# Kernel optimization log

Measured on AMD Instinct MI355X. Metric: run time of the kernel, lower is better.

Reference implementation:

```python
import jax, jax.numpy as jnp
import numpy as np

N_POWER_ITER = 5


def _spectral_normalize(w, n_iter=N_POWER_ITER):
    # w: [out, in] 1x1-conv weight; divide by top singular value (power iteration,
    # deterministic init), mirroring torch.nn.utils.spectral_norm's reparameterization.
    u = jnp.full((w.shape[0],), 1.0 / np.sqrt(w.shape[0]), dtype=w.dtype)
    for _ in range(n_iter):
        v = w.T @ u
        v = v / (jnp.linalg.norm(v) + 1e-12)
        u = w @ v
        u = u / (jnp.linalg.norm(u) + 1e-12)
    sigma = u @ (w @ v)
    return w / sigma


def _maxpool2x2(x):
    # x: [B, C, H, W] -> [B, C, H//2, W//2]
    B, C, H, W = x.shape
    return x.reshape(B, C, H // 2, 2, W // 2, 2).max(axis=(3, 5))


def _conv1x1(w, x):
    # 1x1 conv == channel-mixing einsum. w: [out, in], x: [B, in, H, W]
    return jnp.einsum('oc,bchw->bohw', w, x)


def setup_inputs() -> dict:
    key = jax.random.key(0)
    kx, kq, kk, kv, ko = jax.random.split(key, 5)
    C = 512
    B, H, W = 16, 64, 64
    scale = 0.05
    return {
        'x': jax.random.normal(kx, (B, C, H, W), dtype=jnp.float32),
        'Wq': jax.random.normal(kq, (C // 8, C), dtype=jnp.float32) * scale,
        'Wk': jax.random.normal(kk, (C // 8, C), dtype=jnp.float32) * scale,
        'Wv': jax.random.normal(kv, (C // 2, C), dtype=jnp.float32) * scale,
        'Wo': jax.random.normal(ko, (C, C // 2), dtype=jnp.float32) * scale,
        'gamma': jnp.array([0.5], dtype=jnp.float32),
    }


def reference(x, Wq, Wk, Wv, Wo, gamma):
    B, C, H, W = x.shape
    n_ftrs = H * W
    wq = _spectral_normalize(Wq)
    wk = _spectral_normalize(Wk)
    wv = _spectral_normalize(Wv)
    wo = _spectral_normalize(Wo)
    f = _conv1x1(wq, x).reshape(B, C // 8, n_ftrs)                      # [B, C/8, HW]
    g = _maxpool2x2(_conv1x1(wk, x)).reshape(B, C // 8, n_ftrs // 4)    # [B, C/8, HW/4]
    h = _maxpool2x2(_conv1x1(wv, x)).reshape(B, C // 2, n_ftrs // 4)    # [B, C/2, HW/4]
    # scores: [B, HW, HW/4]; softmax over kv positions
    beta = jax.nn.softmax(jnp.einsum('bcn,bcm->bnm', f, g), axis=-1)
    # attention output: [B, C/2, HW]
    o = jnp.einsum('bcm,bnm->bcn', h, beta).reshape(B, C // 2, H, W)
    o = _conv1x1(wo, o)                                                 # [B, C, H, W]
    return gamma.reshape(()) * o + x
```

## Files before the change

kernel.cpp:

```cpp
#include <hip/hip_runtime.h>
#include <cstdint>

typedef __attribute__((ext_vector_type(8))) short bf16x8;
typedef __attribute__((ext_vector_type(4))) float f32x4;
typedef __attribute__((ext_vector_type(2))) unsigned int u32x2;

#define B_   16
#define C_   512
#define HW_  4096
#define M3_  384
#define HWP_ 1024
#define CV_  256

__device__ __forceinline__ unsigned short f2b(float f) {
  union { float f; unsigned u; } v; v.f = f;
  unsigned r = v.u + 0x7fffu + ((v.u >> 16) & 1u);
  return (unsigned short)(r >> 16);
}
__device__ __forceinline__ float b2f(unsigned short b) {
  union { unsigned u; float f; } v; v.u = ((unsigned)b) << 16;
  return v.f;
}
__device__ __forceinline__ f32x4 mfma16(bf16x8 a, bf16x8 b, f32x4 c) {
  return __builtin_amdgcn_mfma_f32_16x16x32_bf16(a, b, c, 0, 0, 0);
}

__global__ __launch_bounds__(256) void k_transpose(const float* __restrict__ x,
                                                   unsigned short* __restrict__ xb) {
  __shared__ unsigned short t[64][66];
  const int b = blockIdx.z, k0 = blockIdx.y * 64, n0 = blockIdx.x * 64;
  const float* xp = x + (size_t)b * C_ * HW_;
  const int ln = threadIdx.x & 63, g = threadIdx.x >> 6;
  for (int kk = g; kk < 64; kk += 4)
    t[kk][ln] = f2b(xp[(size_t)(k0 + kk) * HW_ + n0 + ln]);
  __syncthreads();
  unsigned short* xo = xb + (size_t)b * HW_ * C_;
  for (int nn = g; nn < 64; nn += 4)
    xo[(size_t)(n0 + nn) * C_ + k0 + ln] = t[ln][nn];
}

__global__ __launch_bounds__(256) void k_wtrans(
    const float* __restrict__ Wq, const float* __restrict__ Wk,
    const float* __restrict__ Wv, const float* __restrict__ Wo,
    float* __restrict__ wt) {
  const float* w; int out, in; float* dst;
  switch (blockIdx.z) {
    case 0: w = Wq; out = 64;  in = 512; dst = wt;          break;
    case 1: w = Wk; out = 64;  in = 512; dst = wt + 32768;  break;
    case 2: w = Wv; out = 256; in = 512; dst = wt + 65536;  break;
    default: w = Wo; out = 512; in = 256; dst = wt + 196608; break;
  }
  const int o0 = blockIdx.y * 64, i0 = blockIdx.x * 64;
  if (o0 >= out || i0 >= in) return;
  __shared__ float t[64][65];
  const int ln = threadIdx.x & 63, g = threadIdx.x >> 6;
  for (int oo = g; oo < 64; oo += 4)
    t[oo][ln] = w[(size_t)(o0 + oo) * in + i0 + ln];
  __syncthreads();
  for (int ii = g; ii < 64; ii += 4)
    dst[(size_t)(i0 + ii) * out + o0 + ln] = t[ln][ii];
}

__device__ __forceinline__ float breduce1024(float val, float* red) {
  __syncthreads();
#pragma unroll
  for (int off = 32; off > 0; off >>= 1) val += __shfl_down(val, off);
  if ((threadIdx.x & 63) == 0) red[threadIdx.x >> 6] = val;
  __syncthreads();
  float s = 0.f;
#pragma unroll
  for (int i = 0; i < 16; ++i) s += red[i];
  return s;
}

__global__ __launch_bounds__(1024) void k_specnorm(
    const float* __restrict__ Wq, const float* __restrict__ Wk,
    const float* __restrict__ Wv, const float* __restrict__ Wo,
    const float* __restrict__ wt,
    unsigned short* __restrict__ wqkv, unsigned short* __restrict__ wob) {
  __shared__ float u[512], v[512];
  __shared__ float part[4096];
  __shared__ float red[16];
  const float* w; const float* wT; int out, in; unsigned short* dst;
  switch (blockIdx.x) {
    case 0: w = Wq; wT = wt;          out = 64;  in = 512; dst = wqkv;             break;
    case 1: w = Wk; wT = wt + 32768;  out = 64;  in = 512; dst = wqkv + 64 * 512;  break;
    case 2: w = Wv; wT = wt + 65536;  out = 256; in = 512; dst = wqkv + 128 * 512; break;
    default: w = Wo; wT = wt + 196608; out = 512; in = 256; dst = wob;             break;
  }
  const int tid = threadIdx.x;
  const float rs = rsqrtf((float)out);
  if (tid < out) u[tid] = rs;
  __syncthreads();
  for (int it = 0; it < 5; ++it) {
    {
      const int G = in >> 2, nch = 1024 / G;
      const int ch = tid / G, grp = tid - ch * G;
      const int rpc = out / nch, obase = ch * rpc;
      f32x4 acc = {0.f, 0.f, 0.f, 0.f};
#pragma unroll 8
      for (int r = 0; r < rpc; ++r) {
        const int o = obase + r;
        const f32x4 wv = *reinterpret_cast<const f32x4*>(&w[(size_t)o * in + grp * 4]);
        const float uo = u[o];
        acc[0] += wv[0] * uo; acc[1] += wv[1] * uo;
        acc[2] += wv[2] * uo; acc[3] += wv[3] * uo;
      }
      *reinterpret_cast<f32x4*>(&part[ch * in + grp * 4]) = acc;
      __syncthreads();
      if (tid < in) {
        float s = 0.f;
        for (int c2 = 0; c2 < nch; ++c2) s += part[c2 * in + tid];
        v[tid] = s;
      }
    }
    {
      float ss = 0.f;
      __syncthreads();
      if (tid < in) ss = v[tid] * v[tid];
      ss = breduce1024(ss, red);
      const float sv = 1.f / (sqrtf(ss) + 1e-12f);
      if (tid < in) v[tid] *= sv;
      __syncthreads();
    }
    {
      const int G = out >> 2, nch = 1024 / G;
      const int ch = tid / G, grp = tid - ch * G;
      const int cpc = in / nch, cbase = ch * cpc;
      f32x4 acc = {0.f, 0.f, 0.f, 0.f};
#pragma unroll 8
      for (int r = 0; r < cpc; ++r) {
        const int c = cbase + r;
        const f32x4 wv = *reinterpret_cast<const f32x4*>(&wT[(size_t)c * out + grp * 4]);
        const float vc = v[c];
        acc[0] += wv[0] * vc; acc[1] += wv[1] * vc;
        acc[2] += wv[2] * vc; acc[3] += wv[3] * vc;
      }
      *reinterpret_cast<f32x4*>(&part[ch * out + grp * 4]) = acc;
      __syncthreads();
      if (tid < out) {
        float s = 0.f;
        for (int c2 = 0; c2 < nch; ++c2) s += part[c2 * out + tid];
        u[tid] = s;
      }
    }
    {
      float su = 0.f;
      __syncthreads();
      if (tid < out) su = u[tid] * u[tid];
      su = breduce1024(su, red);
      const float sv2 = 1.f / (sqrtf(su) + 1e-12f);
      if (tid < out) u[tid] *= sv2;
      __syncthreads();
    }
  }
  float sp = 0.f;
  {
    const int G = out >> 2, nch = 1024 / G;
    const int ch = tid / G, grp = tid - ch * G;
    const int cpc = in / nch, cbase = ch * cpc;
    f32x4 acc = {0.f, 0.f, 0.f, 0.f};
#pragma unroll 8
    for (int r = 0; r < cpc; ++r) {
      const int c = cbase + r;
      const f32x4 wv = *reinterpret_cast<const f32x4*>(&wT[(size_t)c * out + grp * 4]);
      const float vc = v[c];
      acc[0] += wv[0] * vc; acc[1] += wv[1] * vc;
      acc[2] += wv[2] * vc; acc[3] += wv[3] * vc;
    }
    *reinterpret_cast<f32x4*>(&part[ch * out + grp * 4]) = acc;
    __syncthreads();
    if (tid < out) {
      float s = 0.f;
      for (int c2 = 0; c2 < nch; ++c2) s += part[c2 * out + tid];
      sp = s * u[tid];
    }
  }
  sp = breduce1024(sp, red);
  const float oscale = (blockIdx.x == 0) ? 1.44269504f : 1.0f;
  const float inv_sigma = (1.f / sp) * oscale;
  const int total = out * in;
  for (int i = tid * 4; i < total; i += 4096) {
    const f32x4 wv = *reinterpret_cast<const f32x4*>(&w[i]);
    u32x2 pw;
    pw[0] = ((unsigned)f2b(wv[1] * inv_sigma) << 16) | f2b(wv[0] * inv_sigma);
    pw[1] = ((unsigned)f2b(wv[3] * inv_sigma) << 16) | f2b(wv[2] * inv_sigma);
    *reinterpret_cast<u32x2*>(&dst[i]) = pw;
  }
}

__global__ __launch_bounds__(256) void k_gemm_qkv(
    const unsigned short* __restrict__ xb, const unsigned short* __restrict__ wqkv,
    unsigned short* __restrict__ yt) {
  __shared__ alignas(16) char smem[32768];
  unsigned short* As = (unsigned short*)smem;
  unsigned short* Bs = (unsigned short*)(smem + 16384);
  const int lid = blockIdx.x;
  const int swz = (lid & 7) * 192 + (lid >> 3);
  const int mt = swz % 3, rest = swz / 3;
  const int nt = rest & 31, b = rest >> 5;
  const int n0 = nt * 128, m0 = mt * 128;
  const unsigned short* Ap = xb + (size_t)b * HW_ * C_ + (size_t)n0 * C_;
  const unsigned short* Bp = wqkv + (size_t)m0 * C_;
  const int tid = threadIdx.x, lane = tid & 63, wid = tid >> 6;
  const int wn = (wid >> 1) * 64, wm = (wid & 1) * 64;
  f32x4 acc[4][4] = {};
  for (int k0 = 0; k0 < C_; k0 += 64) {
    __syncthreads();
#pragma unroll
    for (int i = 0; i < 4; ++i) {
      const int r = i * 32 + (tid >> 3);
      const int s = tid & 7, ss = s ^ (r & 7);
      *reinterpret_cast<f32x4*>(&As[r * 64 + ss * 8]) =
          *reinterpret_cast<const f32x4*>(&Ap[(size_t)r * C_ + k0 + s * 8]);
      *reinterpret_cast<f32x4*>(&Bs[r * 64 + ss * 8]) =
          *reinterpret_cast<const f32x4*>(&Bp[(size_t)r * C_ + k0 + s * 8]);
    }
    __syncthreads();
#pragma unroll
    for (int kk = 0; kk < 2; ++kk) {
      bf16x8 af[4], bfr[4];
#pragma unroll
      for (int i = 0; i < 4; ++i) {
        const int r = wn + i * 16 + (lane & 15);
        const int slot = (kk * 4 + (lane >> 4)) ^ (r & 7);
        af[i] = *reinterpret_cast<const bf16x8*>(&As[r * 64 + slot * 8]);
      }
#pragma unroll
      for (int j = 0; j < 4; ++j) {
        const int r = wm + j * 16 + (lane & 15);
        const int slot = (kk * 4 + (lane >> 4)) ^ (r & 7);
        bfr[j] = *reinterpret_cast<const bf16x8*>(&Bs[r * 64 + slot * 8]);
      }
#pragma unroll
      for (int i = 0; i < 4; ++i)
#pragma unroll
        for (int j = 0; j < 4; ++j) acc[i][j] = mfma16(af[i], bfr[j], acc[i][j]);
    }
  }
  unsigned short* eps = (unsigned short*)smem;
  unsigned short* Y = yt + (size_t)b * HW_ * M3_;
#pragma unroll
  for (int h = 0; h < 2; ++h) {
    __syncthreads();
    if ((wid >> 1) == h) {
#pragma unroll
      for (int i = 0; i < 4; ++i)
#pragma unroll
        for (int j = 0; j < 4; ++j)
#pragma unroll
          for (int r = 0; r < 4; ++r) {
            const int nl = i * 16 + (lane >> 4) * 4 + r;
            const int ml = wm + j * 16 + (lane & 15);
            eps[nl * 136 + ml] = f2b(acc[i][j][r]);
          }
    }
    __syncthreads();
#pragma unroll
    for (int t = 0; t < 4; ++t) {
      const int row = t * 16 + (tid >> 4);
      const int m8 = (tid & 15) * 8;
      *reinterpret_cast<f32x4*>(&Y[(size_t)(n0 + h * 64 + row) * M3_ + m0 + m8]) =
          *reinterpret_cast<const f32x4*>(&eps[row * 136 + m8]);
    }
  }
}

__global__ __launch_bounds__(256) void k_pool_g(const unsigned short* __restrict__ yt,
                                                unsigned short* __restrict__ gt) {
  const int b = blockIdx.y, mp0 = blockIdx.x * 64;
  const int c = threadIdx.x & 63, dm = threadIdx.x >> 6;
  const unsigned short* Y = yt + (size_t)b * HW_ * M3_;
  unsigned short* G = gt + (size_t)b * HWP_ * 64;
  for (int mm = dm; mm < 64; mm += 4) {
    const int mp = mp0 + mm;
    const int n00 = (mp >> 5) * 128 + (mp & 31) * 2;
    const float a0 = b2f(Y[(size_t)n00 * M3_ + 64 + c]);
    const float a1 = b2f(Y[(size_t)(n00 + 1) * M3_ + 64 + c]);
    const float a2 = b2f(Y[(size_t)(n00 + 64) * M3_ + 64 + c]);
    const float a3 = b2f(Y[(size_t)(n00 + 65) * M3_ + 64 + c]);
    G[(size_t)mp * 64 + c] = f2b(fmaxf(fmaxf(a0, a1), fmaxf(a2, a3)));
  }
}

__global__ __launch_bounds__(256) void k_pool_vt(const unsigned short* __restrict__ yt,
                                                 unsigned short* __restrict__ vt) {
  __shared__ unsigned short t[64][66];
  const int b = blockIdx.z, mp0 = blockIdx.x * 64, cv0 = blockIdx.y * 64;
  const unsigned short* Y = yt + (size_t)b * HW_ * M3_;
  const int c = threadIdx.x & 63, dm = threadIdx.x >> 6;
  for (int mm = dm; mm < 64; mm += 4) {
    const int mp = mp0 + mm;
    const int n00 = (mp >> 5) * 128 + (mp & 31) * 2;
    const float a0 = b2f(Y[(size_t)n00 * M3_ + 128 + cv0 + c]);
    const float a1 = b2f(Y[(size_t)(n00 + 1) * M3_ + 128 + cv0 + c]);
    const float a2 = b2f(Y[(size_t)(n00 + 64) * M3_ + 128 + cv0 + c]);
    const float a3 = b2f(Y[(size_t)(n00 + 65) * M3_ + 128 + cv0 + c]);
    t[mm][c] = f2b(fmaxf(fmaxf(a0, a1), fmaxf(a2, a3)));
  }
  __syncthreads();
  unsigned short* V = vt + (size_t)b * CV_ * HWP_;
  for (int cc = dm; cc < 64; cc += 4)
    V[(size_t)(cv0 + cc) * HWP_ + mp0 + c] = t[c][cc];
}

__global__ __launch_bounds__(256, 2) void k_attn(
    const unsigned short* __restrict__ yt, const unsigned short* __restrict__ gt,
    const unsigned short* __restrict__ vt, unsigned short* __restrict__ oat) {
  __shared__ alignas(16) char smem[57344];
  unsigned short* Ks = (unsigned short*)smem;
  unsigned short* Vs = (unsigned short*)(smem + 8192);
  unsigned short* Ps = (unsigned short*)(smem + 40960);
  const int lid = blockIdx.x;
  const int swz = (lid & 7) * 64 + (lid >> 3);
  const int q0 = (swz & 31) * 128, b = swz >> 5;
  const int tid = threadIdx.x, lane = tid & 63, wid = tid >> 6;
  const int q = lane & 15, g = lane >> 4;
  const unsigned short* Qg = yt + (size_t)b * HW_ * M3_ + (size_t)(q0 + wid * 32) * M3_;
  const unsigned short* Gg = gt + (size_t)b * HWP_ * 64;
  const unsigned short* Vg = vt + (size_t)b * CV_ * HWP_;
  unsigned short* P = Ps + wid * 2048;
  bf16x8 qf[2][2];
#pragma unroll
  for (int h = 0; h < 2; ++h)
#pragma unroll
    for (int kk = 0; kk < 2; ++kk)
      qf[h][kk] = *reinterpret_cast<const bf16x8*>(&Qg[(size_t)(h * 16 + q) * M3_ + kk * 32 + g * 8]);
  f32x4 kreg[2], vreg[8];
#pragma unroll
  for (int t = 0; t < 2; ++t) {
    const int i = tid + t * 256, r = i >> 3, s = i & 7;
    kreg[t] = *reinterpret_cast<const f32x4*>(&Gg[(size_t)r * 64 + s * 8]);
  }
#pragma unroll
  for (int t = 0; t < 8; ++t) {
    const int i = tid + t * 256, r = i >> 3, s = i & 7;
    vreg[t] = *reinterpret_cast<const f32x4*>(&Vg[(size_t)r * HWP_ + s * 8]);
  }
  f32x4 oacc[2][16] = {};
  float m_run[2] = {-1e30f, -1e30f}, l_run[2] = {0.f, 0.f};
  for (int it = 0; it < 16; ++it) {
    __syncthreads();
#pragma unroll
    for (int t = 0; t < 2; ++t) {
      const int i = tid + t * 256, r = i >> 3, s = i & 7, ss = s ^ (r & 7);
      *reinterpret_cast<f32x4*>(&Ks[r * 64 + ss * 8]) = kreg[t];
    }
#pragma unroll
    for (int t = 0; t < 8; ++t) {
      const int i = tid + t * 256, r = i >> 3, s = i & 7, ss = s ^ (r & 7);
      *reinterpret_cast<f32x4*>(&Vs[r * 64 + ss * 8]) = vreg[t];
    }
    __syncthreads();
    if (it < 15) {
      const int kvn = (it + 1) * 64;
#pragma unroll
      for (int t = 0; t < 2; ++t) {
        const int i = tid + t * 256, r = i >> 3, s = i & 7;
        kreg[t] = *reinterpret_cast<const f32x4*>(&Gg[(size_t)(kvn + r) * 64 + s * 8]);
      }
#pragma unroll
      for (int t = 0; t < 8; ++t) {
        const int i = tid + t * 256, r = i >> 3, s = i & 7;
        vreg[t] = *reinterpret_cast<const f32x4*>(&Vg[(size_t)r * HWP_ + kvn + s * 8]);
      }
    }
    f32x4 sacc[2][4] = {};
#pragma unroll
    for (int kk = 0; kk < 2; ++kk) {
      bf16x8 kf[4];
#pragma unroll
      for (int i = 0; i < 4; ++i) {
        const int row = i * 16 + q;
        const int sl = (kk * 4 + g) ^ (row & 7);
        kf[i] = *reinterpret_cast<const bf16x8*>(&Ks[row * 64 + sl * 8]);
      }
#pragma unroll
      for (int h = 0; h < 2; ++h)
#pragma unroll
        for (int i = 0; i < 4; ++i) sacc[h][i] = mfma16(kf[i], qf[h][kk], sacc[h][i]);
    }
#pragma unroll
    for (int h = 0; h < 2; ++h) {
      float tmax = -1e30f;
#pragma unroll
      for (int i = 0; i < 4; ++i)
#pragma unroll
        for (int r = 0; r < 4; ++r) tmax = fmaxf(tmax, sacc[h][i][r]);
      tmax = fmaxf(tmax, __shfl_xor(tmax, 16));
      tmax = fmaxf(tmax, __shfl_xor(tmax, 32));
      if (__any(tmax > m_run[h] + 11.0f)) {
        const float mnew = fmaxf(m_run[h], tmax);
        const float alpha = exp2f(m_run[h] - mnew);
        m_run[h] = mnew;
        l_run[h] *= alpha;
        float al[4];
#pragma unroll
        for (int r = 0; r < 4; ++r) al[r] = __shfl(alpha, g * 4 + r);
#pragma unroll
        for (int j = 0; j < 16; ++j) {
          oacc[h][j][0] *= al[0]; oacc[h][j][1] *= al[1];
          oacc[h][j][2] *= al[2]; oacc[h][j][3] *= al[3];
        }
      }
      const int qg = h * 16 + q;
      float lsum = 0.f;
#pragma unroll
      for (int i = 0; i < 4; ++i) {
        const float p0 = exp2f(sacc[h][i][0] - m_run[h]);
        const float p1 = exp2f(sacc[h][i][1] - m_run[h]);
        const float p2 = exp2f(sacc[h][i][2] - m_run[h]);
        const float p3 = exp2f(sacc[h][i][3] - m_run[h]);
        lsum += (p0 + p1) + (p2 + p3);
        u32x2 pw;
        pw[0] = ((unsigned)f2b(p1) << 16) | f2b(p0);
        pw[1] = ((unsigned)f2b(p3) << 16) | f2b(p2);
        const int sl = (2 * i + (g >> 1)) ^ (qg & 7);
        *reinterpret_cast<u32x2*>(&P[qg * 64 + sl * 8 + (g & 1) * 4]) = pw;
      }
      lsum += __shfl_xor(lsum, 16);
      lsum += __shfl_xor(lsum, 32);
      l_run[h] += lsum;
    }
    __builtin_amdgcn_s_setprio(1);
#pragma unroll
    for (int kk = 0; kk < 2; ++kk) {
      bf16x8 pa[2];
#pragma unroll
      for (int h = 0; h < 2; ++h)
        pa[h] = *reinterpret_cast<const bf16x8*>(
            &P[(h * 16 + q) * 64 + (((kk * 4 + g) ^ (q & 7))) * 8]);
#pragma unroll
      for (int j = 0; j < 16; ++j) {
        const int row = j * 16 + q;
        const int sl = (kk * 4 + g) ^ (row & 7);
        const bf16x8 vf = *reinterpret_cast<const bf16x8*>(&Vs[row * 64 + sl * 8]);
        oacc[0][j] = mfma16(pa[0], vf, oacc[0][j]);
        oacc[1][j] = mfma16(pa[1], vf, oacc[1][j]);
      }
    }
    __builtin_amdgcn_s_setprio(0);
  }
  float linv[2][4];
#pragma unroll
  for (int h = 0; h < 2; ++h) {
    const float myinv = 1.f / l_run[h];
#pragma unroll
    for (int r = 0; r < 4; ++r) linv[h][r] = __shfl(myinv, g * 4 + r);
  }
  unsigned short* eps = (unsigned short*)smem;
  unsigned short* O = oat + (size_t)b * HW_ * CV_ + (size_t)q0 * CV_;
#pragma unroll
  for (int ch = 0; ch < 2; ++ch) {
    __syncthreads();
    if ((wid >> 1) == ch) {
#pragma unroll
      for (int h = 0; h < 2; ++h)
#pragma unroll
        for (int j = 0; j < 16; ++j)
#pragma unroll
          for (int r = 0; r < 4; ++r) {
            const int row = (wid & 1) * 32 + h * 16 + g * 4 + r;
            const int cv = j * 16 + q;
            eps[row * 264 + cv] = f2b(oacc[h][j][r] * linv[h][r]);
          }
    }
    __syncthreads();
#pragma unroll
    for (int t = 0; t < 8; ++t) {
      const int row = t * 8 + (tid >> 5);
      const int cv8 = (tid & 31) * 8;
      *reinterpret_cast<f32x4*>(&O[(size_t)(ch * 64 + row) * CV_ + cv8]) =
          *reinterpret_cast<const f32x4*>(&eps[row * 264 + cv8]);
    }
  }
}

__global__ __launch_bounds__(256) void k_gemm_out(
    const unsigned short* __restrict__ oat, const unsigned short* __restrict__ wob,
    const float* __restrict__ x, const float* __restrict__ gamma,
    float* __restrict__ out) {
  __shared__ alignas(16) char smem[32768];
  unsigned short* As = (unsigned short*)smem;
  unsigned short* Bs = (unsigned short*)(smem + 16384);
  const int lid = blockIdx.x;
  const int swz = (lid & 7) * 256 + (lid >> 3);
  const int ct = swz & 3, nt = (swz >> 2) & 31, b = swz >> 7;
  const int n0 = nt * 128, co0 = ct * 128;
  const unsigned short* Ap = wob + (size_t)co0 * CV_;
  const unsigned short* Bp = oat + (size_t)b * HW_ * CV_ + (size_t)n0 * CV_;
  const int tid = threadIdx.x, lane = tid & 63, wid = tid >> 6;
  const int wc = (wid >> 1) * 64, wn = (wid & 1) * 64;
  f32x4 acc[4][4] = {};
  for (int k0 = 0; k0 < CV_; k0 += 64) {
    __syncthreads();
#pragma unroll
    for (int i = 0; i < 4; ++i) {
      const int r = i * 32 + (tid >> 3);
      const int s = tid & 7, ss = s ^ (r & 7);
      *reinterpret_cast<f32x4*>(&As[r * 64 + ss * 8]) =
          *reinterpret_cast<const f32x4*>(&Ap[(size_t)r * CV_ + k0 + s * 8]);
      *reinterpret_cast<f32x4*>(&Bs[r * 64 + ss * 8]) =
          *reinterpret_cast<const f32x4*>(&Bp[(size_t)r * CV_ + k0 + s * 8]);
    }
    __syncthreads();
#pragma unroll
    for (int kk = 0; kk < 2; ++kk) {
      bf16x8 af[4], bfr[4];
#pragma unroll
      for (int i = 0; i < 4; ++i) {
        const int r = wc + i * 16 + (lane & 15);
        const int slot = (kk * 4 + (lane >> 4)) ^ (r & 7);
        af[i] = *reinterpret_cast<const bf16x8*>(&As[r * 64 + slot * 8]);
      }
#pragma unroll
      for (int j = 0; j < 4; ++j) {
        const int r = wn + j * 16 + (lane & 15);
        const int slot = (kk * 4 + (lane >> 4)) ^ (r & 7);
        bfr[j] = *reinterpret_cast<const bf16x8*>(&Bs[r * 64 + slot * 8]);
      }
#pragma unroll
      for (int i = 0; i < 4; ++i)
#pragma unroll
        for (int j = 0; j < 4; ++j) acc[i][j] = mfma16(af[i], bfr[j], acc[i][j]);
    }
  }
  float* eps = (float*)smem;
  const float g = gamma[0];
  const size_t base = (size_t)b * C_ * HW_;
#pragma unroll
  for (int h = 0; h < 4; ++h) {
    __syncthreads();
    if ((wid >> 1) == (h >> 1)) {
#pragma unroll
      for (int ii = 0; ii < 2; ++ii) {
        const int i = (h & 1) * 2 + ii;
#pragma unroll
        for (int j = 0; j < 4; ++j)
#pragma unroll
          for (int r = 0; r < 4; ++r) {
            const int col2 = ii * 16 + (lane >> 4) * 4 + r;
            const int nl = wn + j * 16 + (lane & 15);
            eps[col2 * 132 + nl] = acc[i][j][r];
          }
      }
    }
    __syncthreads();
#pragma unroll
    for (int t = 0; t < 4; ++t) {
      const int row = t * 8 + (tid >> 5);
      const int col = (tid & 31) * 4;
      const size_t goff = base + (size_t)(co0 + h * 32 + row) * HW_ + n0 + col;
      const f32x4 xv = *reinterpret_cast<const f32x4*>(&x[goff]);
      const f32x4 av = *reinterpret_cast<const f32x4*>(&eps[row * 132 + col]);
      f32x4 ov;
      ov[0] = g * av[0] + xv[0];
      ov[1] = g * av[1] + xv[1];
      ov[2] = g * av[2] + xv[2];
      ov[3] = g * av[3] + xv[3];
      *reinterpret_cast<f32x4*>(&out[goff]) = ov;
    }
  }
}

extern "C" void kernel_launch(void* const* d_in, const int* in_sizes, int n_in,
                              void* d_out, int out_size, void* d_ws, size_t ws_size,
                              hipStream_t stream) {
  (void)in_sizes; (void)n_in; (void)out_size; (void)ws_size;
  const float* x     = (const float*)d_in[0];
  const float* Wq    = (const float*)d_in[1];
  const float* Wk    = (const float*)d_in[2];
  const float* Wv    = (const float*)d_in[3];
  const float* Wo    = (const float*)d_in[4];
  const float* gamma = (const float*)d_in[5];
  float* out = (float*)d_out;
  char* ws = (char*)d_ws;

  unsigned short* wqkv = (unsigned short*)(ws);
  unsigned short* wob  = (unsigned short*)(ws + 393216);
  unsigned short* xb   = (unsigned short*)(ws + 655360);
  unsigned short* yt   = (unsigned short*)(ws + 67764224);
  unsigned short* gt   = (unsigned short*)(ws + 118095872);
  unsigned short* vt   = (unsigned short*)(ws + 120193024);
  unsigned short* oat  = xb;
  float* wt = (float*)yt;

  k_transpose<<<dim3(64, 8, 16), 256, 0, stream>>>(x, xb);
  k_wtrans<<<dim3(8, 8, 4), 256, 0, stream>>>(Wq, Wk, Wv, Wo, wt);
  k_specnorm<<<4, 1024, 0, stream>>>(Wq, Wk, Wv, Wo, wt, wqkv, wob);
  k_gemm_qkv<<<1536, 256, 0, stream>>>(xb, wqkv, yt);
  k_pool_g<<<dim3(16, 16), 256, 0, stream>>>(yt, gt);
  k_pool_vt<<<dim3(16, 4, 16), 256, 0, stream>>>(yt, vt);
  k_attn<<<512, 256, 0, stream>>>(yt, gt, vt, oat);
  k_gemm_out<<<2048, 256, 0, stream>>>(oat, wob, x, gamma, out);
}
```

Before: 323.8 us.

## Double-buffer K/V tiles in LDS with 32-wide KV blocks in attention

The attention kernel now processes 32 KV positions per iteration instead of 64 and keeps two LDS buffers for K and V. The next tile is written to the alternate buffer while the current one is consumed, which removes one of the two barriers per iteration. The goal is to overlap LDS staging with MFMA work and to shrink shared memory and register footprint. In exchange it runs twice as many iterations, so the per-iteration softmax bookkeeping and barrier overhead is paid twice as often.

```diff
diff --git a/kernel.cpp b/kernel.cpp
--- a/kernel.cpp
+++ b/kernel.cpp
@@ -307,10 +307,7 @@
 __global__ __launch_bounds__(256, 2) void k_attn(
     const unsigned short* __restrict__ yt, const unsigned short* __restrict__ gt,
     const unsigned short* __restrict__ vt, unsigned short* __restrict__ oat) {
-  __shared__ alignas(16) char smem[57344];
-  unsigned short* Ks = (unsigned short*)smem;
-  unsigned short* Vs = (unsigned short*)(smem + 8192);
-  unsigned short* Ps = (unsigned short*)(smem + 40960);
+  __shared__ alignas(16) char smem[49152];
   const int lid = blockIdx.x;
   const int swz = (lid & 7) * 64 + (lid >> 3);
   const int q0 = (swz & 31) * 128, b = swz >> 5;
@@ -319,72 +316,83 @@
   const unsigned short* Qg = yt + (size_t)b * HW_ * M3_ + (size_t)(q0 + wid * 32) * M3_;
   const unsigned short* Gg = gt + (size_t)b * HWP_ * 64;
   const unsigned short* Vg = vt + (size_t)b * CV_ * HWP_;
-  unsigned short* P = Ps + wid * 2048;
+  unsigned short* P = (unsigned short*)(smem + 40960) + wid * 1024;
   bf16x8 qf[2][2];
 #pragma unroll
   for (int h = 0; h < 2; ++h)
 #pragma unroll
     for (int kk = 0; kk < 2; ++kk)
       qf[h][kk] = *reinterpret_cast<const bf16x8*>(&Qg[(size_t)(h * 16 + q) * M3_ + kk * 32 + g * 8]);
-  f32x4 kreg[2], vreg[8];
-#pragma unroll
-  for (int t = 0; t < 2; ++t) {
-    const int i = tid + t * 256, r = i >> 3, s = i & 7;
-    kreg[t] = *reinterpret_cast<const f32x4*>(&Gg[(size_t)r * 64 + s * 8]);
-  }
-#pragma unroll
-  for (int t = 0; t < 8; ++t) {
-    const int i = tid + t * 256, r = i >> 3, s = i & 7;
+  const int kr = tid >> 3, ks = tid & 7;
+  f32x4 kreg, vreg[4];
+  kreg = *reinterpret_cast<const f32x4*>(&Gg[(size_t)kr * 64 + ks * 8]);
+#pragma unroll
+  for (int t = 0; t < 4; ++t) {
+    const int i = tid + t * 256, r = i >> 2, s = i & 3;
     vreg[t] = *reinterpret_cast<const f32x4*>(&Vg[(size_t)r * HWP_ + s * 8]);
   }
+  {
+    unsigned short* Kb = (unsigned short*)smem;
+    unsigned short* Vb = (unsigned short*)(smem + 8192);
+    *reinterpret_cast<f32x4*>(&Kb[kr * 64 + (ks ^ (kr & 7)) * 8]) = kreg;
+#pragma unroll
+    for (int t = 0; t < 4; ++t) {
+      const int i = tid + t * 256, r = i >> 2, s = i & 3;
+      *reinterpret_cast<f32x4*>(&Vb[r * 32 + (s ^ (r & 3)) * 8]) = vreg[t];
+    }
+  }
+  kreg = *reinterpret_cast<const f32x4*>(&Gg[(size_t)(32 + kr) * 64 + ks * 8]);
+#pragma unroll
+  for (int t = 0; t < 4; ++t) {
+    const int i = tid + t * 256, r = i >> 2, s = i & 3;
+    vreg[t] = *reinterpret_cast<const f32x4*>(&Vg[(size_t)r * HWP_ + 32 + s * 8]);
+  }
+  __syncthreads();
   f32x4 oacc[2][16] = {};
   float m_run[2] = {-1e30f, -1e30f}, l_run[2] = {0.f, 0.f};
-  for (int it = 0; it < 16; ++it) {
-    __syncthreads();
-#pragma unroll
-    for (int t = 0; t < 2; ++t) {
-      const int i = tid + t * 256, r = i >> 3, s = i & 7, ss = s ^ (r & 7);
-      *reinterpret_cast<f32x4*>(&Ks[r * 64 + ss * 8]) = kreg[t];
-    }
-#pragma unroll
-    for (int t = 0; t < 8; ++t) {
-      const int i = tid + t * 256, r = i >> 3, s = i & 7, ss = s ^ (r & 7);
-      *reinterpret_cast<f32x4*>(&Vs[r * 64 + ss * 8]) = vreg[t];
-    }
-    __syncthreads();
-    if (it < 15) {
-      const int kvn = (it + 1) * 64;
-#pragma unroll
-      for (int t = 0; t < 2; ++t) {
-        const int i = tid + t * 256, r = i >> 3, s = i & 7;
-        kreg[t] = *reinterpret_cast<const f32x4*>(&Gg[(size_t)(kvn + r) * 64 + s * 8]);
-      }
-#pragma unroll
-      for (int t = 0; t < 8; ++t) {
-        const int i = tid + t * 256, r = i >> 3, s = i & 7;
+  for (int it = 0; it < 32; ++it) {
+    const int cur = it & 1;
+    unsigned short* Kc = (unsigned short*)(smem + cur * 4096);
+    unsigned short* Vc = (unsigned short*)(smem + 8192 + cur * 16384);
+    if (it < 31) {
+      unsigned short* Kn = (unsigned short*)(smem + (cur ^ 1) * 4096);
+      unsigned short* Vn = (unsigned short*)(smem + 8192 + (cur ^ 1) * 16384);
+      *reinterpret_cast<f32x4*>(&Kn[kr * 64 + (ks ^ (kr & 7)) * 8]) = kreg;
+#pragma unroll
+      for (int t = 0; t < 4; ++t) {
+        const int i = tid + t * 256, r = i >> 2, s = i & 3;
+        *reinterpret_cast<f32x4*>(&Vn[r * 32 + (s ^ (r & 3)) * 8]) = vreg[t];
+      }
+    }
+    if (it < 30) {
+      const int kvn = (it + 2) * 32;
+      kreg = *reinterpret_cast<const f32x4*>(&Gg[(size_t)(kvn + kr) * 64 + ks * 8]);
+#pragma unroll
+      for (int t = 0; t < 4; ++t) {
+        const int i = tid + t * 256, r = i >> 2, s = i & 3;
         vreg[t] = *reinterpret_cast<const f32x4*>(&Vg[(size_t)r * HWP_ + kvn + s * 8]);
       }
     }
-    f32x4 sacc[2][4] = {};
+    f32x4 sacc[2][2] = {};
 #pragma unroll
     for (int kk = 0; kk < 2; ++kk) {
-      bf16x8 kf[4];
-#pragma unroll
-      for (int i = 0; i < 4; ++i) {
+      bf16x8 kf[2];
+#pragma unroll
+      for (int i = 0; i < 2; ++i) {
         const int row = i * 16 + q;
         const int sl = (kk * 4 + g) ^ (row & 7);
-        kf[i] = *reinterpret_cast<const bf16x8*>(&Ks[row * 64 + sl * 8]);
+        kf[i] = *reinterpret_cast<const bf16x8*>(&Kc[row * 64 + sl * 8]);
       }
 #pragma unroll
       for (int h = 0; h < 2; ++h)
 #pragma unroll
-        for (int i = 0; i < 4; ++i) sacc[h][i] = mfma16(kf[i], qf[h][kk], sacc[h][i]);
+        for (int i = 0; i < 2; ++i) sacc[h][i] = mfma16(kf[i], qf[h][kk], sacc[h][i]);
     }
 #pragma unroll
     for (int h = 0; h < 2; ++h) {
       float tmax = -1e30f;
 #pragma unroll
-      for (int i = 0; i < 4; ++i)
+      for (int i = 0; i < 2; ++i)
 #pragma unroll
         for (int r = 0; r < 4; ++r) tmax = fmaxf(tmax, sacc[h][i][r]);
       tmax = fmaxf(tmax, __shfl_xor(tmax, 16));
@@ -406,7 +414,7 @@
       const int qg = h * 16 + q;
       float lsum = 0.f;
 #pragma unroll
-      for (int i = 0; i < 4; ++i) {
+      for (int i = 0; i < 2; ++i) {
         const float p0 = exp2f(sacc[h][i][0] - m_run[h]);
         const float p1 = exp2f(sacc[h][i][1] - m_run[h]);
         const float p2 = exp2f(sacc[h][i][2] - m_run[h]);
@@ -415,31 +423,30 @@
         u32x2 pw;
         pw[0] = ((unsigned)f2b(p1) << 16) | f2b(p0);
         pw[1] = ((unsigned)f2b(p3) << 16) | f2b(p2);
-        const int sl = (2 * i + (g >> 1)) ^ (qg & 7);
-        *reinterpret_cast<u32x2*>(&P[qg * 64 + sl * 8 + (g & 1) * 4]) = pw;
+        const int c = 2 * i + (g >> 1);
+        *reinterpret_cast<u32x2*>(&P[qg * 32 + ((c ^ (qg & 3)) * 8) + (g & 1) * 4]) = pw;
       }
       lsum += __shfl_xor(lsum, 16);
       lsum += __shfl_xor(lsum, 32);
       l_run[h] += lsum;
     }
     __builtin_amdgcn_s_setprio(1);
-#pragma unroll
-    for (int kk = 0; kk < 2; ++kk) {
-      bf16x8 pa[2];
-#pragma unroll
-      for (int h = 0; h < 2; ++h)
-        pa[h] = *reinterpret_cast<const bf16x8*>(
-            &P[(h * 16 + q) * 64 + (((kk * 4 + g) ^ (q & 7))) * 8]);
-#pragma unroll
-      for (int j = 0; j < 16; ++j) {
-        const int row = j * 16 + q;
-        const int sl = (kk * 4 + g) ^ (row & 7);
-        const bf16x8 vf = *reinterpret_cast<const bf16x8*>(&Vs[row * 64 + sl * 8]);
-        oacc[0][j] = mfma16(pa[0], vf, oacc[0][j]);
-        oacc[1][j] = mfma16(pa[1], vf, oacc[1][j]);
-      }
+    bf16x8 pa[2];
+#pragma unroll
+    for (int h = 0; h < 2; ++h) {
+      const int qg = h * 16 + q;
+      pa[h] = *reinterpret_cast<const bf16x8*>(&P[qg * 32 + ((g ^ (qg & 3)) * 8)]);
+    }
+#pragma unroll
+    for (int j = 0; j < 16; ++j) {
+      const int row = j * 16 + q;
+      const int sl = g ^ (row & 3);
+      const bf16x8 vf = *reinterpret_cast<const bf16x8*>(&Vc[row * 32 + sl * 8]);
+      oacc[0][j] = mfma16(pa[0], vf, oacc[0][j]);
+      oacc[1][j] = mfma16(pa[1], vf, oacc[1][j]);
     }
     __builtin_amdgcn_s_setprio(0);
+    __syncthreads();
   }
   float linv[2][4];
 #pragma unroll
```

After: 296.3 us. -8.5%, faster.
